# Kernel optimization log

Hardware: AMD Instinct MI355X
Metric: run time of the kernel (lower is better)

## Reference

```python
import jax, jax.numpy as jnp
import numpy as np

N = 100_000      # nodes
E = 2_500_000    # edges (nnz), avg degree 25
D_IN = 32
D_OUT = 32


def setup_inputs() -> dict:
    key = jax.random.key(0)
    k1, k2, k3, k4 = jax.random.split(key, 4)
    X = jax.random.normal(k1, (N, D_IN), dtype=jnp.float32)
    # CSR row offsets: sorted, anchored at 0 and E
    rp = jnp.sort(jax.random.randint(k2, (N + 1,), 0, E, dtype=jnp.int32))
    rp = rp.at[0].set(0).at[-1].set(E)
    ci = jax.random.randint(k3, (E,), 0, N, dtype=jnp.int32)
    W = (jax.random.normal(k4, (D_IN, D_OUT), dtype=jnp.float32)
         * (1.0 / np.sqrt(D_OUT)).astype(np.float32))
    dummy = jnp.zeros((1,), dtype=jnp.int32)
    return {
        "X": X,
        "weights": W,
        "row_pointers": rp,
        "column_index": ci,
        "blockPartition": dummy,
        "edgeToColumn": dummy,
        "edgeToRow": dummy,
        "hybrid_type": dummy,
        "row_nzr": dummy,
        "col_nzr": dummy,
    }


def reference(X, weights, row_pointers, column_index, blockPartition,
              edgeToColumn, edgeToRow, hybrid_type, row_nzr, col_nzr):
    # Fused GIN: X_prime = A @ X (CSR neighbor sum), then X_prime @ W.
    # Recover per-edge destination row from CSR offsets: row r owns edges
    # in [row_pointers[r], row_pointers[r+1]).
    edge_ids = jnp.arange(E, dtype=row_pointers.dtype)
    row = jnp.searchsorted(row_pointers, edge_ids, side="right") - 1  # [E]
    gathered = X[column_index]                       # [E, D_IN] (irregular gather)
    X_prime = jax.ops.segment_sum(gathered, row, num_segments=N)  # [N, D_IN]
    return X_prime @ weights                          # [N, D_OUT]
```

## Files before the change

kernel.cpp:

```cpp
#include <hip/hip_runtime.h>

#define D 32

__global__ __launch_bounds__(256, 8)
void xw_kernel(const float* __restrict__ X, const float* __restrict__ W,
               float* __restrict__ Y, int n) {
    const int lane = threadIdx.x & 63;
    const int j    = lane & 31;
    const int wid  = blockIdx.x * (blockDim.x >> 6) + (threadIdx.x >> 6);
    const int nw   = gridDim.x * (blockDim.x >> 6);

    float w[D];
    #pragma unroll
    for (int d = 0; d < D; ++d) w[d] = W[d * D + j];

    for (int r = wid; r <= n; r += nw) {
        float o0 = 0.f, o1 = 0.f;
        if (r < n) {
            const float* xr =
                X + (size_t)(unsigned)__builtin_amdgcn_readfirstlane(r) * D;
            #pragma unroll
            for (int d = 0; d < D; d += 2) {
                o0 = fmaf(xr[d],     w[d],     o0);
                o1 = fmaf(xr[d + 1], w[d + 1], o1);
            }
        }
        if (lane < 32) Y[(size_t)r * D + j] = o0 + o1;
    }
}

template <int K>
__device__ __forceinline__ void gather_acc(const float* __restrict__ Y,
                                           int myci, int base, int g, int s,
                                           float4& acc) {
    float4 x[K];
    #pragma unroll
    for (int it = 0; it < K; ++it) {
        int c = __shfl(myci, (base + it) * 8 + g, 64);
        x[it] = ((const float4*)(Y + (size_t)(unsigned)c * D))[s];
    }
    #pragma unroll
    for (int it = 0; it < K; ++it) {
        acc.x += x[it].x; acc.y += x[it].y;
        acc.z += x[it].z; acc.w += x[it].w;
    }
}

__global__ __launch_bounds__(256, 8)
void agg_kernel(const float* __restrict__ Y, const int* __restrict__ rp,
                const int* __restrict__ ci, float* __restrict__ out, int n) {
    const int tid  = threadIdx.x;
    const int wave = tid >> 6;
    const int lane = tid & 63;
    int row = blockIdx.x * 4 + wave;
    if (row >= n) return;
    row = __builtin_amdgcn_readfirstlane(row);

    const int start = rp[row];
    const int deg   = rp[row + 1] - start;

    const int g  = lane >> 3;
    const int s  = lane & 7;
    const int zr = n;

    float4 acc = make_float4(0.f, 0.f, 0.f, 0.f);

    for (int cb = 0; cb < deg; cb += 64) {
        const int rem  = deg - cb;
        const int nv   = rem < 64 ? rem : 64;
        const int myci = (lane < nv) ? ci[start + cb + lane] : zr;

        switch ((nv + 7) >> 3) {
            case 1: gather_acc<1>(Y, myci, 0, g, s, acc); break;
            case 2: gather_acc<2>(Y, myci, 0, g, s, acc); break;
            case 3: gather_acc<3>(Y, myci, 0, g, s, acc); break;
            case 4: gather_acc<4>(Y, myci, 0, g, s, acc); break;
            case 5: gather_acc<4>(Y, myci, 0, g, s, acc);
                    gather_acc<1>(Y, myci, 4, g, s, acc); break;
            case 6: gather_acc<4>(Y, myci, 0, g, s, acc);
                    gather_acc<2>(Y, myci, 4, g, s, acc); break;
            case 7: gather_acc<4>(Y, myci, 0, g, s, acc);
                    gather_acc<3>(Y, myci, 4, g, s, acc); break;
            default: gather_acc<4>(Y, myci, 0, g, s, acc);
                     gather_acc<4>(Y, myci, 4, g, s, acc); break;
        }
    }

    #pragma unroll
    for (int off = 8; off < 64; off <<= 1) {
        acc.x += __shfl_xor(acc.x, off, 64);
        acc.y += __shfl_xor(acc.y, off, 64);
        acc.z += __shfl_xor(acc.z, off, 64);
        acc.w += __shfl_xor(acc.w, off, 64);
    }
    if (lane < 8) ((float4*)(out + (size_t)row * D))[s] = acc;
}

__global__ __launch_bounds__(256, 4)
void gin_fused(const float* __restrict__ X,
               const float* __restrict__ W,
               const int* __restrict__ rp,
               const int* __restrict__ ci,
               float* __restrict__ out,
               int n) {
    __shared__ float Wl[D * D];

    int tid = threadIdx.x;
    {
        const float4* Wv = (const float4*)W;
        float4* Wlv = (float4*)Wl;
        Wlv[tid] = Wv[tid];
    }
    __syncthreads();

    int wave = tid >> 6;
    int lane = tid & 63;
    int row = blockIdx.x * 4 + wave;
    if (row >= n) return;

    int start = rp[row];
    int deg   = rp[row + 1] - start;

    int g = lane >> 3;
    int s = lane & 7;

    float4 acc = make_float4(0.f, 0.f, 0.f, 0.f);

    for (int cb = 0; cb < deg; cb += 64) {
        int rem = deg - cb;
        int nv  = rem < 64 ? rem : 64;
        int myci = (lane < nv) ? ci[start + cb + lane] : 0;
        {
            float4 x[4]; float m[4];
            #pragma unroll
            for (int it = 0; it < 4; ++it) {
                int l = it * 8 + g;
                int c = __shfl(myci, l, 64);
                m[it] = (l < rem) ? 1.f : 0.f;
                x[it] = ((const float4*)(X + (size_t)c * D))[s];
            }
            #pragma unroll
            for (int it = 0; it < 4; ++it) {
                acc.x = fmaf(m[it], x[it].x, acc.x);
                acc.y = fmaf(m[it], x[it].y, acc.y);
                acc.z = fmaf(m[it], x[it].z, acc.z);
                acc.w = fmaf(m[it], x[it].w, acc.w);
            }
        }
        if (rem > 32) {
            float4 x[4]; float m[4];
            #pragma unroll
            for (int it = 0; it < 4; ++it) {
                int l = (it + 4) * 8 + g;
                int c = __shfl(myci, l, 64);
                m[it] = (l < rem) ? 1.f : 0.f;
                x[it] = ((const float4*)(X + (size_t)c * D))[s];
            }
            #pragma unroll
            for (int it = 0; it < 4; ++it) {
                acc.x = fmaf(m[it], x[it].x, acc.x);
                acc.y = fmaf(m[it], x[it].y, acc.y);
                acc.z = fmaf(m[it], x[it].z, acc.z);
                acc.w = fmaf(m[it], x[it].w, acc.w);
            }
        }
    }

    #pragma unroll
    for (int off = 8; off < 64; off <<= 1) {
        acc.x += __shfl_xor(acc.x, off, 64);
        acc.y += __shfl_xor(acc.y, off, 64);
        acc.z += __shfl_xor(acc.z, off, 64);
        acc.w += __shfl_xor(acc.w, off, 64);
    }

    int j = lane & 31;
    float o = 0.f;
    #pragma unroll
    for (int sg = 0; sg < 8; ++sg) {
        float ax = __shfl(acc.x, sg, 64);
        float ay = __shfl(acc.y, sg, 64);
        float az = __shfl(acc.z, sg, 64);
        float aw = __shfl(acc.w, sg, 64);
        int d = 4 * sg;
        o = fmaf(ax, Wl[(d    ) * D + j], o);
        o = fmaf(ay, Wl[(d + 1) * D + j], o);
        o = fmaf(az, Wl[(d + 2) * D + j], o);
        o = fmaf(aw, Wl[(d + 3) * D + j], o);
    }
    if (lane < 32) out[(size_t)row * D + j] = o;
}

extern "C" void kernel_launch(void* const* d_in, const int* in_sizes, int n_in,
                              void* d_out, int out_size, void* d_ws, size_t ws_size,
                              hipStream_t stream) {
    const float* X  = (const float*)d_in[0];
    const float* W  = (const float*)d_in[1];
    const int*   rp = (const int*)d_in[2];
    const int*   ci = (const int*)d_in[3];
    float* out = (float*)d_out;

    int n = in_sizes[2] - 1;
    size_t ybytes = (size_t)(n + 1) * D * sizeof(float);

    if (ws_size >= ybytes) {
        float* Y = (float*)d_ws;
        hipLaunchKernelGGL(xw_kernel, dim3(1024), dim3(256), 0, stream,
                           X, W, Y, n);
        hipLaunchKernelGGL(agg_kernel, dim3((n + 3) / 4), dim3(256), 0, stream,
                           Y, rp, ci, out, n);
    } else {
        hipLaunchKernelGGL(gin_fused, dim3((n + 3) / 4), dim3(256), 0, stream,
                           X, W, rp, ci, out, n);
    }
}
```

Baseline: 132.8 us.

## Make aggregation kernel persistent with prefetch of next row's CSR data

The aggregation kernel becomes a grid-stride persistent kernel capped at 2048 blocks, where each wave processes many rows. While it gathers the current row, it prefetches the next row's row pointers and first 64 column indices, which hides that index-load latency behind the gather work. The cost is more live registers and lower memory-level parallelism from fewer in-flight waves, and load balance across waves with uneven degrees may get worse. The diff also leaves a leftover no-op block in the code.

```diff
diff --git a/kernel.cpp b/kernel.cpp
--- a/kernel.cpp
+++ b/kernel.cpp
@@ -46,54 +46,84 @@
     }
 }
 
+__device__ __forceinline__ void ladder(const float* __restrict__ Y, int myci,
+                                       int nv, int g, int s, float4& acc) {
+    switch ((nv + 7) >> 3) {
+        case 1: gather_acc<1>(Y, myci, 0, g, s, acc); break;
+        case 2: gather_acc<2>(Y, myci, 0, g, s, acc); break;
+        case 3: gather_acc<3>(Y, myci, 0, g, s, acc); break;
+        case 4: gather_acc<4>(Y, myci, 0, g, s, acc); break;
+        case 5: gather_acc<4>(Y, myci, 0, g, s, acc);
+                gather_acc<1>(Y, myci, 4, g, s, acc); break;
+        case 6: gather_acc<4>(Y, myci, 0, g, s, acc);
+                gather_acc<2>(Y, myci, 4, g, s, acc); break;
+        case 7: gather_acc<4>(Y, myci, 0, g, s, acc);
+                gather_acc<3>(Y, myci, 4, g, s, acc); break;
+        default: gather_acc<4>(Y, myci, 0, g, s, acc);
+                 gather_acc<4>(Y, myci, 4, g, s, acc); break;
+    }
+}
+
 __global__ __launch_bounds__(256, 8)
 void agg_kernel(const float* __restrict__ Y, const int* __restrict__ rp,
                 const int* __restrict__ ci, float* __restrict__ out, int n) {
-    const int tid  = threadIdx.x;
-    const int wave = tid >> 6;
-    const int lane = tid & 63;
-    int row = blockIdx.x * 4 + wave;
-    if (row >= n) return;
-    row = __builtin_amdgcn_readfirstlane(row);
-
-    const int start = rp[row];
-    const int deg   = rp[row + 1] - start;
-
+    const int lane = threadIdx.x & 63;
     const int g  = lane >> 3;
     const int s  = lane & 7;
     const int zr = n;
 
-    float4 acc = make_float4(0.f, 0.f, 0.f, 0.f);
-
-    for (int cb = 0; cb < deg; cb += 64) {
-        const int rem  = deg - cb;
-        const int nv   = rem < 64 ? rem : 64;
-        const int myci = (lane < nv) ? ci[start + cb + lane] : zr;
-
-        switch ((nv + 7) >> 3) {
-            case 1: gather_acc<1>(Y, myci, 0, g, s, acc); break;
-            case 2: gather_acc<2>(Y, myci, 0, g, s, acc); break;
-            case 3: gather_acc<3>(Y, myci, 0, g, s, acc); break;
-            case 4: gather_acc<4>(Y, myci, 0, g, s, acc); break;
-            case 5: gather_acc<4>(Y, myci, 0, g, s, acc);
-                    gather_acc<1>(Y, myci, 4, g, s, acc); break;
-            case 6: gather_acc<4>(Y, myci, 0, g, s, acc);
-                    gather_acc<2>(Y, myci, 4, g, s, acc); break;
-            case 7: gather_acc<4>(Y, myci, 0, g, s, acc);
-                    gather_acc<3>(Y, myci, 4, g, s, acc); break;
-            default: gather_acc<4>(Y, myci, 0, g, s, acc);
-                     gather_acc<4>(Y, myci, 4, g, s, acc); break;
-        }
-    }
-
-    #pragma unroll
-    for (int off = 8; off < 64; off <<= 1) {
-        acc.x += __shfl_xor(acc.x, off, 64);
-        acc.y += __shfl_xor(acc.y, off, 64);
-        acc.z += __shfl_xor(acc.z, off, 64);
-        acc.w += __shfl_xor(acc.w, off, 64);
-    }
-    if (lane < 8) ((float4*)(out + (size_t)row * D))[s] = acc;
+    const int wid = (blockIdx.x * blockDim.x + threadIdx.x) >> 6;
+    const int nw  = (gridDim.x * blockDim.x) >> 6;
+
+    int r = __builtin_amdgcn_readfirstlane(wid);
+    if (r >= n) return;
+
+    int start = rp[r];
+    int end   = rp[r + 1];
+    {
+        int nv0 = end - start; nv0 = nv0 > 64 ? 64 : nv0;
+        start = start;
+    }
+    int nv0 = end - start; nv0 = nv0 > 64 ? 64 : nv0;
+    int myci = (lane < nv0) ? ci[start + lane] : zr;
+
+    while (true) {
+        const int deg = end - start;
+        const int rn  = r + nw;
+        const bool has_next = rn < n;
+
+        int nstart = 0, nend = 0, next_ci = zr;
+        if (has_next) {
+            nstart = rp[rn];
+            nend   = rp[rn + 1];
+            int nnv = nend - nstart; nnv = nnv > 64 ? 64 : nnv;
+            next_ci = (lane < nnv) ? ci[nstart + lane] : zr;
+        }
+
+        float4 acc = make_float4(0.f, 0.f, 0.f, 0.f);
+        if (deg > 0) {
+            int nv = deg > 64 ? 64 : deg;
+            ladder(Y, myci, nv, g, s, acc);
+            for (int cb = 64; cb < deg; cb += 64) {
+                int rem = deg - cb;
+                int nv2 = rem > 64 ? 64 : rem;
+                int c2  = (lane < nv2) ? ci[start + cb + lane] : zr;
+                ladder(Y, c2, nv2, g, s, acc);
+            }
+        }
+
+        #pragma unroll
+        for (int off = 8; off < 64; off <<= 1) {
+            acc.x += __shfl_xor(acc.x, off, 64);
+            acc.y += __shfl_xor(acc.y, off, 64);
+            acc.z += __shfl_xor(acc.z, off, 64);
+            acc.w += __shfl_xor(acc.w, off, 64);
+        }
+        if (lane < 8) ((float4*)(out + (size_t)r * D))[s] = acc;
+
+        if (!has_next) break;
+        r = rn; start = nstart; end = nend; myci = next_ci;
+    }
 }
 
 __global__ __launch_bounds__(256, 4)
@@ -207,7 +237,9 @@
         float* Y = (float*)d_ws;
         hipLaunchKernelGGL(xw_kernel, dim3(1024), dim3(256), 0, stream,
                            X, W, Y, n);
-        hipLaunchKernelGGL(agg_kernel, dim3((n + 3) / 4), dim3(256), 0, stream,
+        int nwaves = (n + 3) / 4;
+        int blocks = nwaves < 2048 ? nwaves : 2048;
+        hipLaunchKernelGGL(agg_kernel, dim3(blocks), dim3(256), 0, stream,
                            Y, rp, ci, out, n);
     } else {
         hipLaunchKernelGGL(gin_fused, dim3((n + 3) / 4), dim3(256), 0, stream,
```

Result: no change. 132.9 us (+0.1%).
